# Performance work log

Measured on AMD Instinct MI355X. Metric: run time of the kernel, lower is better.

The kernel has to match this reference:

```python
import jax, jax.numpy as jnp
import numpy as np

B, N, DIM = 16, 2048, 256  # dim = 8 * win_length (win_length=32)


def setup_inputs() -> dict:
    key = jax.random.key(0)
    k_x, k_w, k_b = jax.random.split(key, 3)
    x = jax.random.normal(k_x, (B, N, DIM), dtype=jnp.float32)
    # nn.Linear(dim, dim): y = x @ W.T + b
    W_q = jax.random.normal(k_w, (DIM, DIM), dtype=jnp.float32) / np.sqrt(DIM)
    b_q = jax.random.normal(k_b, (DIM,), dtype=jnp.float32) * 0.01
    return {"input": x, "W_q": W_q, "b_q": b_q}


def reference(input, W_q, b_q):
    # Linear projection (dropout is identity in eval mode)
    p = jnp.einsum("bnd,ed->bne", input, W_q) + b_q  # [B, N, DIM]
    # Pairwise cosine similarity: normalize once, then one Gram matmul.
    # This is exactly dot(p_i, p_j) / (sqrt(dot(p_i,p_i)) * sqrt(dot(p_j,p_j)))
    # from the original nested-loop implementation.
    norm = jnp.sqrt(jnp.sum(p * p, axis=-1, keepdims=True))  # [B, N, 1]
    pn = p / norm
    attn_raw = jnp.einsum("bnd,bmd->bnm", pn, pn)  # [B, N, N], symmetric
    return attn_raw
```

## Files before the change

### kernel.cpp

```cpp
#include <hip/hip_runtime.h>
#include <hip/hip_bf16.h>


typedef __bf16 bf16x8 __attribute__((ext_vector_type(8)));
typedef float  f32x4  __attribute__((ext_vector_type(4)));

__device__ __forceinline__ void gl_lds16(const void* g, void* l) {
  __builtin_amdgcn_global_load_lds((const __attribute__((address_space(1))) void*)g,
                                   (__attribute__((address_space(3))) void*)l, 16, 0, 0);
}

__device__ __forceinline__ bf16x8 pack8(f32x4 a, f32x4 b) {
  bf16x8 r;
  r[0] = (__bf16)a[0]; r[1] = (__bf16)a[1]; r[2] = (__bf16)a[2]; r[3] = (__bf16)a[3];
  r[4] = (__bf16)b[0]; r[5] = (__bf16)b[1]; r[6] = (__bf16)b[2]; r[7] = (__bf16)b[3];
  return r;
}

__global__ __launch_bounds__(512, 1) void proj_kernel(
    const float* __restrict__ x, const float* __restrict__ W,
    const float* __restrict__ bq, __bf16* __restrict__ pn) {
  __shared__ __attribute__((aligned(16))) char ldsW[131072];
  const int t = threadIdx.x;
  const int lane = t & 63;
  const int w = t >> 6;

  #pragma unroll
  for (int it = 0; it < 16; ++it) {
    int base = (it * 512 + t) * 8;
    int row  = base >> 8;
    int colb = (base & 255) * 2;
    f32x4 v0 = *(const f32x4*)(W + base);
    f32x4 v1 = *(const f32x4*)(W + base + 4);
    *(bf16x8*)(ldsW + row * 512 + (colb ^ ((row & 7) << 4))) = pack8(v0, v1);
  }
  __syncthreads();

  const int r0 = blockIdx.x * 128 + w * 16;
  const int arow = r0 + (lane & 15);
  const float* xrow = x + (size_t)arow * 256 + (lane >> 4) * 8;
  bf16x8 afr[8];
  #pragma unroll
  for (int kk = 0; kk < 8; ++kk) {
    f32x4 v0 = *(const f32x4*)(xrow + kk * 32);
    f32x4 v1 = *(const f32x4*)(xrow + kk * 32 + 4);
    afr[kk] = pack8(v0, v1);
  }

  f32x4 acc[16];
  #pragma unroll
  for (int ct = 0; ct < 16; ++ct) acc[ct] = (f32x4){0.f, 0.f, 0.f, 0.f};
  const int kb0 = (lane >> 4) * 16;
  #pragma unroll
  for (int ct = 0; ct < 16; ++ct) {
    int brow = ct * 16 + (lane & 15);
    const char* wb = ldsW + brow * 512;
    int sw = (brow & 7) << 4;
    #pragma unroll
    for (int kk = 0; kk < 8; ++kk) {
      bf16x8 bf = *(const bf16x8*)(wb + ((kk * 64 + kb0) ^ sw));
      acc[ct] = __builtin_amdgcn_mfma_f32_16x16x32_bf16(afr[kk], bf, acc[ct], 0, 0, 0);
    }
  }

  float bc[16];
  #pragma unroll
  for (int ct = 0; ct < 16; ++ct) bc[ct] = bq[ct * 16 + (lane & 15)];
  #pragma unroll
  for (int ct = 0; ct < 16; ++ct) {
    #pragma unroll
    for (int r = 0; r < 4; ++r) acc[ct][r] += bc[ct];
  }
  #pragma unroll
  for (int r = 0; r < 4; ++r) {
    float s = 0.f;
    #pragma unroll
    for (int ct = 0; ct < 16; ++ct) s += acc[ct][r] * acc[ct][r];
    s += __shfl_xor(s, 1); s += __shfl_xor(s, 2);
    s += __shfl_xor(s, 4); s += __shfl_xor(s, 8);
    float rn = rsqrtf(s);
    int rowg = r0 + (lane >> 4) * 4 + r;
    __bf16* dst = pn + (size_t)rowg * 256 + (lane & 15);
    #pragma unroll
    for (int ct = 0; ct < 16; ++ct) dst[ct * 16] = (__bf16)(acc[ct][r] * rn);
  }
}

__global__ __launch_bounds__(512, 1) void gram_kernel(
    const __bf16* __restrict__ pn, float* __restrict__ out) {
  __shared__ __attribute__((aligned(16))) char lds[131072];
  const int t = threadIdx.x;
  const int lane = t & 63;
  const int w = t >> 6;
  const int bid = blockIdx.x;
  const int batch = bid >> 8;
  const int ti = (bid >> 4) & 15;
  const int tj = bid & 15;
  const char* pb = (const char*)(pn + (size_t)batch * 2048 * 256);

  #pragma unroll
  for (int i = 0; i < 8; ++i) {
    int off = ((w * 8 + i) * 64 + lane) * 16;
    int row = off >> 9;
    int kb  = off & 511;
    gl_lds16(pb + (size_t)(ti * 128 + row) * 512 + (kb ^ ((row & 7) << 4)),
             lds + (w * 8 + i) * 1024);
  }
  #pragma unroll
  for (int i = 0; i < 8; ++i) {
    int off = ((w * 8 + i) * 64 + lane) * 16;
    int row = off >> 9;
    int kb  = off & 511;
    gl_lds16(pb + (size_t)(tj * 128 + row) * 512 + (kb ^ ((row & 7) << 4)),
             lds + 65536 + (w * 8 + i) * 1024);
  }
  asm volatile("s_waitcnt vmcnt(0)" ::: "memory");
  __syncthreads();

  const int wr = w >> 2;
  const int wc = w & 3;
  f32x4 acc[4][2];
  #pragma unroll
  for (int m = 0; m < 4; ++m)
    #pragma unroll
    for (int n = 0; n < 2; ++n) acc[m][n] = (f32x4){0.f, 0.f, 0.f, 0.f};

  const int la0 = wr * 64 + (lane & 15);
  const int lb0 = wc * 32 + (lane & 15);
  const int kb0 = (lane >> 4) * 16;
  const char* ldsA = lds;
  const char* ldsB = lds + 65536;
  #pragma unroll
  for (int kk = 0; kk < 8; ++kk) {
    int kb = kk * 64 + kb0;
    bf16x8 a[4], bfr[2];
    #pragma unroll
    for (int m = 0; m < 4; ++m) {
      int row = la0 + m * 16;
      a[m] = *(const bf16x8*)(ldsA + row * 512 + (kb ^ ((row & 7) << 4)));
    }
    #pragma unroll
    for (int n = 0; n < 2; ++n) {
      int row = lb0 + n * 16;
      bfr[n] = *(const bf16x8*)(ldsB + row * 512 + (kb ^ ((row & 7) << 4)));
    }
    #pragma unroll
    for (int m = 0; m < 4; ++m)
      #pragma unroll
      for (int n = 0; n < 2; ++n)
        acc[m][n] = __builtin_amdgcn_mfma_f32_16x16x32_bf16(a[m], bfr[n], acc[m][n], 0, 0, 0);
  }

  float* ob = out + (size_t)batch * 2048 * 2048;
  const int ro0 = ti * 128 + wr * 64 + (lane >> 4) * 4;
  const int co0 = tj * 128 + wc * 32 + (lane & 15);
  #pragma unroll
  for (int m = 0; m < 4; ++m)
    #pragma unroll
    for (int n = 0; n < 2; ++n)
      #pragma unroll
      for (int r = 0; r < 4; ++r)
        ob[(size_t)(ro0 + m * 16 + r) * 2048 + (co0 + n * 16)] = acc[m][n][r];
}

extern "C" void kernel_launch(void* const* d_in, const int* in_sizes, int n_in,
                              void* d_out, int out_size, void* d_ws, size_t ws_size,
                              hipStream_t stream) {
  const float* x  = (const float*)d_in[0];
  const float* Wq = (const float*)d_in[1];
  const float* bq = (const float*)d_in[2];
  float* out = (float*)d_out;
  __bf16* pn = (__bf16*)d_ws;

  proj_kernel<<<dim3(256), dim3(512), 0, stream>>>(x, Wq, bq, pn);
  gram_kernel<<<dim3(4096), dim3(512), 0, stream>>>(pn, out);
}
```

Measured before the change: 333.6 us.

## Restructure gram kernel into persistent stripes with double-buffered B tiles

The gram kernel now runs 512 blocks, each keeping a 128-row A stripe in registers and walking 16 column tiles of 64 rows over half of N. The next B tile is loaded into a double-buffered LDS region while the current one is computed, and output goes out through nontemporal stores. LDS shrinks to 64KB and launch bounds allow 4 blocks per CU, aiming to overlap loads with MFMA and output writes and to stop re-launching 4096 blocks that each reload A. The risks are fewer blocks for load balancing and an extra syncthreads per tile. The kernel stays heavily bound by output writes (256MB of fp32).

```diff
diff --git a/kernel.cpp b/kernel.cpp
--- a/kernel.cpp
+++ b/kernel.cpp
@@ -86,81 +86,102 @@
   }
 }
 
-__global__ __launch_bounds__(512, 1) void gram_kernel(
+__global__ __launch_bounds__(512, 4) void gram_kernel(
     const __bf16* __restrict__ pn, float* __restrict__ out) {
-  __shared__ __attribute__((aligned(16))) char lds[131072];
+  __shared__ __attribute__((aligned(16))) char lds[65536];
   const int t = threadIdx.x;
   const int lane = t & 63;
   const int w = t >> 6;
+  const int wr = w >> 1;
+  const int wc = w & 1;
   const int bid = blockIdx.x;
-  const int batch = bid >> 8;
-  const int ti = (bid >> 4) & 15;
-  const int tj = bid & 15;
+  const int batch = bid >> 5;
+  const int stripe = (bid >> 1) & 15;
+  const int jhalf = bid & 1;
   const char* pb = (const char*)(pn + (size_t)batch * 2048 * 256);
+  const int i0 = stripe * 128;
+  const int kb0 = (lane >> 4) * 16;
 
   #pragma unroll
   for (int i = 0; i < 8; ++i) {
-    int off = ((w * 8 + i) * 64 + lane) * 16;
+    int off = (i * 512 + t) * 16;
     int row = off >> 9;
     int kb  = off & 511;
-    gl_lds16(pb + (size_t)(ti * 128 + row) * 512 + (kb ^ ((row & 7) << 4)),
-             lds + (w * 8 + i) * 1024);
+    gl_lds16(pb + (size_t)(i0 + row) * 512 + (kb ^ ((row & 7) << 4)),
+             lds + i * 8192 + w * 1024);
   }
+  __syncthreads();
+
+  bf16x8 afr[2][8];
   #pragma unroll
-  for (int i = 0; i < 8; ++i) {
-    int off = ((w * 8 + i) * 64 + lane) * 16;
+  for (int fr = 0; fr < 2; ++fr) {
+    int row = wr * 32 + fr * 16 + (lane & 15);
+    const char* ab = lds + row * 512;
+    int sw = (row & 7) << 4;
+    #pragma unroll
+    for (int kk = 0; kk < 8; ++kk)
+      afr[fr][kk] = *(const bf16x8*)(ab + ((kk * 64 + kb0) ^ sw));
+  }
+  __syncthreads();
+
+  const int jbase = jhalf * 1024;
+  float* ob = out + (size_t)batch * 2048 * 2048;
+  const int ro0 = i0 + wr * 32 + (lane >> 4) * 4;
+
+  #pragma unroll
+  for (int i = 0; i < 4; ++i) {
+    int off = (i * 512 + t) * 16;
     int row = off >> 9;
     int kb  = off & 511;
-    gl_lds16(pb + (size_t)(tj * 128 + row) * 512 + (kb ^ ((row & 7) << 4)),
-             lds + 65536 + (w * 8 + i) * 1024);
+    gl_lds16(pb + (size_t)(jbase + row) * 512 + (kb ^ ((row & 7) << 4)),
+             lds + i * 8192 + w * 1024);
   }
-  asm volatile("s_waitcnt vmcnt(0)" ::: "memory");
   __syncthreads();
 
-  const int wr = w >> 2;
-  const int wc = w & 3;
-  f32x4 acc[4][2];
-  #pragma unroll
-  for (int m = 0; m < 4; ++m)
+  for (int jj = 0; jj < 16; ++jj) {
+    const char* buf = lds + (jj & 1) * 32768;
+    if (jj < 15) {
+      char* nb = lds + ((jj + 1) & 1) * 32768;
+      int j0 = jbase + (jj + 1) * 64;
+      #pragma unroll
+      for (int i = 0; i < 4; ++i) {
+        int off = (i * 512 + t) * 16;
+        int row = off >> 9;
+        int kb  = off & 511;
+        gl_lds16(pb + (size_t)(j0 + row) * 512 + (kb ^ ((row & 7) << 4)),
+                 nb + i * 8192 + w * 1024);
+      }
+    }
+    f32x4 acc[2][2];
     #pragma unroll
-    for (int n = 0; n < 2; ++n) acc[m][n] = (f32x4){0.f, 0.f, 0.f, 0.f};
-
-  const int la0 = wr * 64 + (lane & 15);
-  const int lb0 = wc * 32 + (lane & 15);
-  const int kb0 = (lane >> 4) * 16;
-  const char* ldsA = lds;
-  const char* ldsB = lds + 65536;
-  #pragma unroll
-  for (int kk = 0; kk < 8; ++kk) {
-    int kb = kk * 64 + kb0;
-    bf16x8 a[4], bfr[2];
+    for (int m = 0; m < 2; ++m)
+      #pragma unroll
+      for (int n = 0; n < 2; ++n) acc[m][n] = (f32x4){0.f, 0.f, 0.f, 0.f};
     #pragma unroll
-    for (int m = 0; m < 4; ++m) {
-      int row = la0 + m * 16;
-      a[m] = *(const bf16x8*)(ldsA + row * 512 + (kb ^ ((row & 7) << 4)));
+    for (int kk = 0; kk < 8; ++kk) {
+      bf16x8 bfr[2];
+      #pragma unroll
+      for (int n = 0; n < 2; ++n) {
+        int row = wc * 32 + n * 16 + (lane & 15);
+        bfr[n] = *(const bf16x8*)(buf + row * 512 + ((kk * 64 + kb0) ^ ((row & 7) << 4)));
+      }
+      #pragma unroll
+      for (int m = 0; m < 2; ++m)
+        #pragma unroll
+        for (int n = 0; n < 2; ++n)
+          acc[m][n] = __builtin_amdgcn_mfma_f32_16x16x32_bf16(afr[m][kk], bfr[n], acc[m][n], 0, 0, 0);
     }
+    __syncthreads();
+    int co0 = jbase + jj * 64 + wc * 32 + (lane & 15);
     #pragma unroll
-    for (int n = 0; n < 2; ++n) {
-      int row = lb0 + n * 16;
-      bfr[n] = *(const bf16x8*)(ldsB + row * 512 + (kb ^ ((row & 7) << 4)));
-    }
-    #pragma unroll
-    for (int m = 0; m < 4; ++m)
+    for (int m = 0; m < 2; ++m)
       #pragma unroll
       for (int n = 0; n < 2; ++n)
-        acc[m][n] = __builtin_amdgcn_mfma_f32_16x16x32_bf16(a[m], bfr[n], acc[m][n], 0, 0, 0);
+        #pragma unroll
+        for (int r = 0; r < 4; ++r)
+          __builtin_nontemporal_store(acc[m][n][r],
+              &ob[(size_t)(ro0 + m * 16 + r) * 2048 + (co0 + n * 16)]);
   }
-
-  float* ob = out + (size_t)batch * 2048 * 2048;
-  const int ro0 = ti * 128 + wr * 64 + (lane >> 4) * 4;
-  const int co0 = tj * 128 + wc * 32 + (lane & 15);
-  #pragma unroll
-  for (int m = 0; m < 4; ++m)
-    #pragma unroll
-    for (int n = 0; n < 2; ++n)
-      #pragma unroll
-      for (int r = 0; r < 4; ++r)
-        ob[(size_t)(ro0 + m * 16 + r) * 2048 + (co0 + n * 16)] = acc[m][n][r];
 }
 
 extern "C" void kernel_launch(void* const* d_in, const int* in_sizes, int n_in,
@@ -173,5 +194,5 @@
   __bf16* pn = (__bf16*)d_ws;
 
   proj_kernel<<<dim3(256), dim3(512), 0, stream>>>(x, Wq, bq, pn);
-  gram_kernel<<<dim3(4096), dim3(512), 0, stream>>>(pn, out);
+  gram_kernel<<<dim3(512), dim3(512), 0, stream>>>(pn, out);
 }
```

Result: slower. 350.6 us (+5.1%).
